# Performance work log

Measured on AMD Instinct MI355X. Metric: run time of the kernel, lower is better.

The kernel has to match this reference:

```python
import jax, jax.numpy as jnp
from jax import lax
import numpy as np

MB, N, QST, EPS = 512, 25, 11, 1e-5

def _coords():
    i = np.arange(25)
    # faithful to python3 true division: (i/5 - 2)/2.0, (i%5 - 2)/2.0
    c = np.stack([(i / 5 - 2) / 2.0, (i % 5 - 2) / 2.0], axis=-1).astype(np.float32)
    return jnp.asarray(c)  # [25, 2]

def _conv_bn(x, w, b, g, beta):
    # Conv2d(k=3, stride=2, pad=1) -> ReLU -> BatchNorm (training-mode batch stats)
    y = lax.conv_general_dilated(x, w, (2, 2), [(1, 1), (1, 1)],
                                 dimension_numbers=('NCHW', 'OIHW', 'NCHW'))
    y = jax.nn.relu(y + b[None, :, None, None])
    mean = y.mean(axis=(0, 2, 3), keepdims=True)
    var = y.var(axis=(0, 2, 3), keepdims=True)
    return (y - mean) * jax.lax.rsqrt(var + EPS) * g[None, :, None, None] + beta[None, :, None, None]

def setup_inputs() -> dict:
    key = jax.random.key(0)
    ks = jax.random.split(key, 20)
    w = lambda k, s: jax.random.normal(k, s, jnp.float32) * 0.05
    inp = {
        'img': jax.random.normal(ks[0], (MB, 3, 75, 75), jnp.float32),
        'qst': jax.random.normal(ks[1], (MB, QST), jnp.float32),
        'c1w': w(ks[2], (24, 3, 3, 3)),  'c1b': jnp.zeros((24,)), 'bn1g': jnp.ones((24,)), 'bn1b': jnp.zeros((24,)),
        'c2w': w(ks[3], (24, 24, 3, 3)), 'c2b': jnp.zeros((24,)), 'bn2g': jnp.ones((24,)), 'bn2b': jnp.zeros((24,)),
        'c3w': w(ks[4], (24, 24, 3, 3)), 'c3b': jnp.zeros((24,)), 'bn3g': jnp.ones((24,)), 'bn3b': jnp.zeros((24,)),
        'c4w': w(ks[5], (24, 24, 3, 3)), 'c4b': jnp.zeros((24,)), 'bn4g': jnp.ones((24,)), 'bn4b': jnp.zeros((24,)),
        'gw1': w(ks[6], (256, 63)),  'gb1': jnp.zeros((256,)),
        'gw2': w(ks[7], (256, 256)), 'gb2': jnp.zeros((256,)),
        'gw3': w(ks[8], (256, 256)), 'gb3': jnp.zeros((256,)),
        'gw4': w(ks[9], (256, 256)), 'gb4': jnp.zeros((256,)),
        'fw1': w(ks[10], (256, 256)), 'fb1': jnp.zeros((256,)),
        'fw2': w(ks[11], (256, 256)), 'fb2': jnp.zeros((256,)),
        'fw3': w(ks[12], (10, 256)),  'fb3': jnp.zeros((10,)),
    }
    return inp

def reference(img, qst, c1w, c1b, bn1g, bn1b, c2w, c2b, bn2g, bn2b,
              c3w, c3b, bn3g, bn3b, c4w, c4b, bn4g, bn4b,
              gw1, gb1, gw2, gb2, gw3, gb3, gw4, gb4,
              fw1, fb1, fw2, fb2, fw3, fb3):
    x = _conv_bn(img, c1w, c1b, bn1g, bn1b)
    x = _conv_bn(x, c2w, c2b, bn2g, bn2b)
    x = _conv_bn(x, c3w, c3b, bn3g, bn3b)
    x = _conv_bn(x, c4w, c4b, bn4g, bn4b)  # [mb, 24, 5, 5]
    mb, C = x.shape[0], x.shape[1]
    n = x.shape[2] * x.shape[3]
    xf = x.reshape(mb, C, n).transpose(0, 2, 1)              # [mb, N, 24]
    coord = jnp.broadcast_to(_coords()[None], (mb, n, 2))
    xf = jnp.concatenate([xf, coord], axis=-1)               # [mb, N, 26]
    qrep = jnp.broadcast_to(qst[:, None, :], (mb, n, QST))
    xj = jnp.concatenate([xf, qrep], axis=-1)                # [mb, N, 37]
    # pair[b,a,c] = [xf[b,c], xf[b,a], qst[b]]  (x_i varies over axis 2, x_j over axis 1)
    pair = jnp.concatenate([
        jnp.broadcast_to(xf[:, None, :, :], (mb, n, n, xf.shape[-1])),
        jnp.broadcast_to(xj[:, :, None, :], (mb, n, n, xj.shape[-1])),
    ], axis=-1)                                              # [mb, N, N, 63]
    h = pair.reshape(mb * n * n, -1)
    for w, b in ((gw1, gb1), (gw2, gb2), (gw3, gb3), (gw4, gb4)):
        h = jax.nn.relu(h @ w.T + b)
    xg = h.reshape(mb, n * n, 256).sum(axis=1)               # sum pooling over pairs
    y = jax.nn.relu(xg @ fw1.T + fb1)
    y = jax.nn.relu(y @ fw2.T + fb2)   # dropout treated as identity (eval mode)
    y = y @ fw3.T + fb3
    return jax.nn.log_softmax(y, axis=-1)
```

## Files before the change

kernel.cpp:

```cpp
#include <hip/hip_runtime.h>

typedef __bf16 bf16_t;
typedef __bf16 bf16x8 __attribute__((ext_vector_type(8)));
typedef __bf16 bf16x4 __attribute__((ext_vector_type(4)));
typedef float f32x16 __attribute__((ext_vector_type(16)));

#define MB 512
#define GROWS 128
#define GT_PER_B 5

__global__ __launch_bounds__(256, 2) void conv1_bn(const float* __restrict__ img,
                                                   const float* __restrict__ wT,
                                                   const float* __restrict__ bias,
                                                   float* __restrict__ out,
                                                   float* __restrict__ statsOut)
{
    __shared__ float in_s[3 * 39 * 77];
    __shared__ float red[48];
    int bid = blockIdx.x;
    int n = bid >> 1, tile = bid & 1;
    int oh0 = tile * 19;
    int tid = threadIdx.x;

    for (int idx = tid; idx < 3 * 39 * 77; idx += 256) {
        int ci = idx / (39 * 77);
        int rem = idx - ci * (39 * 77);
        int r = rem / 77, c = rem - r * 77;
        int ih = 2 * oh0 - 1 + r, iw = c - 1;
        float v = 0.f;
        if ((unsigned)ih < 75u && (unsigned)iw < 75u)
            v = img[((n * 3 + ci) * 75 + ih) * 75 + iw];
        in_s[idx] = v;
    }
    __syncthreads();

    int cg = tid >> 6, lane = tid & 63, co0 = cg * 6;
    int off[12];
    bool pv[12];
#pragma unroll
    for (int j = 0; j < 12; ++j) {
        int p = lane + j * 64;
        pv[j] = p < 722;
        int pc = pv[j] ? p : 0;
        int r0 = pc / 38, c0 = pc - r0 * 38;
        off[j] = (r0 * 2) * 77 + c0 * 2;
    }
    float acc[6][12];
#pragma unroll
    for (int c = 0; c < 6; ++c)
#pragma unroll
        for (int j = 0; j < 12; ++j) acc[c][j] = 0.f;

#pragma unroll 1
    for (int ci = 0; ci < 3; ++ci) {
        const float* ip = in_s + ci * (39 * 77);
        const float* wp = wT + ci * 9 * 24 + co0;
#pragma unroll
        for (int kh = 0; kh < 3; ++kh) {
#pragma unroll
            for (int kw = 0; kw < 3; ++kw) {
                float iv[12];
#pragma unroll
                for (int j = 0; j < 12; ++j) iv[j] = ip[off[j] + kh * 77 + kw];
                const float* wr = wp + (kh * 3 + kw) * 24;
                float2 w01 = *(const float2*)(wr);
                float2 w23 = *(const float2*)(wr + 2);
                float2 w45 = *(const float2*)(wr + 4);
#pragma unroll
                for (int j = 0; j < 12; ++j) {
                    acc[0][j] = fmaf(iv[j], w01.x, acc[0][j]);
                    acc[1][j] = fmaf(iv[j], w01.y, acc[1][j]);
                    acc[2][j] = fmaf(iv[j], w23.x, acc[2][j]);
                    acc[3][j] = fmaf(iv[j], w23.y, acc[3][j]);
                    acc[4][j] = fmaf(iv[j], w45.x, acc[4][j]);
                    acc[5][j] = fmaf(iv[j], w45.y, acc[5][j]);
                }
            }
        }
    }

    float sst[6], sq[6];
#pragma unroll
    for (int c = 0; c < 6; ++c) { sst[c] = 0.f; sq[c] = 0.f; }
#pragma unroll
    for (int c = 0; c < 6; ++c) {
        float bv = bias[co0 + c];
#pragma unroll
        for (int j = 0; j < 12; ++j) {
            if (pv[j]) {
                int p = lane + j * 64;
                int r = p / 38, q = p - r * 38;
                float v = fmaxf(acc[c][j] + bv, 0.f);
                out[((n * 24 + co0 + c) * 38 + oh0 + r) * 38 + q] = v;
                sst[c] += v; sq[c] += v * v;
            }
        }
    }
#pragma unroll
    for (int o = 1; o < 64; o <<= 1) {
#pragma unroll
        for (int c = 0; c < 6; ++c) {
            sst[c] += __shfl_xor(sst[c], o);
            sq[c]  += __shfl_xor(sq[c], o);
        }
    }
    if (lane == 0) {
#pragma unroll
        for (int c = 0; c < 6; ++c) {
            red[(co0 + c) * 2]     = sst[c];
            red[(co0 + c) * 2 + 1] = sq[c];
        }
    }
    __syncthreads();
    if (tid < 48) atomicAdd(&statsOut[tid], red[tid]);
}

template <int HIN, int WIN, int HOUT, int WOUT, int OHT, int NP>
__global__ __launch_bounds__(256, 2) void conv24_bn(const float* __restrict__ in,
                                                    const float* __restrict__ wT,
                                                    const float* __restrict__ bias,
                                                    const float* __restrict__ statsIn,
                                                    const float* __restrict__ gIn,
                                                    const float* __restrict__ bIn, float invcntIn,
                                                    float* __restrict__ out,
                                                    float* __restrict__ statsOut, int tilesPerImg)
{
    constexpr int IR = 2 * OHT + 1;
    constexpr int ICW = 2 * WOUT + 1;
    __shared__ float in_s[24 * IR * ICW];
    __shared__ float aff[48];
    __shared__ float red[48];

    int bid = blockIdx.x;
    int n = bid / tilesPerImg, tile = bid - n * tilesPerImg;
    int oh0 = tile * OHT;
    int tid = threadIdx.x;

    if (tid < 24) {
        float mean = statsIn[tid * 2] * invcntIn;
        float var  = statsIn[tid * 2 + 1] * invcntIn - mean * mean;
        float s    = gIn[tid] * rsqrtf(var + 1e-5f);
        aff[tid * 2] = s;
        aff[tid * 2 + 1] = bIn[tid] - mean * s;
    }
    __syncthreads();
    for (int idx = tid; idx < 24 * IR * ICW; idx += 256) {
        int ci = idx / (IR * ICW);
        int rem = idx - ci * (IR * ICW);
        int r = rem / ICW, c = rem - r * ICW;
        int ih = 2 * oh0 - 1 + r, iw = c - 1;
        float v = 0.f;
        if ((unsigned)ih < (unsigned)HIN && (unsigned)iw < (unsigned)WIN)
            v = aff[ci * 2] * in[((n * 24 + ci) * HIN + ih) * WIN + iw] + aff[ci * 2 + 1];
        in_s[idx] = v;
    }
    __syncthreads();

    int cg = tid >> 6, lane = tid & 63, co0 = cg * 6;
    int nvr = HOUT - oh0; if (nvr > OHT) nvr = OHT;
    int nposv = nvr * WOUT;
    int off[NP];
    bool pv[NP];
#pragma unroll
    for (int j = 0; j < NP; ++j) {
        int p = lane + j * 64;
        pv[j] = p < nposv;
        int pc = pv[j] ? p : 0;
        int r0 = pc / WOUT, c0 = pc - r0 * WOUT;
        off[j] = (r0 * 2) * ICW + c0 * 2;
    }
    float acc[6][NP];
#pragma unroll
    for (int c = 0; c < 6; ++c)
#pragma unroll
        for (int j = 0; j < NP; ++j) acc[c][j] = 0.f;

#pragma unroll 1
    for (int ci = 0; ci < 24; ++ci) {
        const float* ip = in_s + ci * (IR * ICW);
        const float* wp = wT + ci * 9 * 24 + co0;
#pragma unroll
        for (int kh = 0; kh < 3; ++kh) {
#pragma unroll
            for (int kw = 0; kw < 3; ++kw) {
                float iv[NP];
#pragma unroll
                for (int j = 0; j < NP; ++j) iv[j] = ip[off[j] + kh * ICW + kw];
                const float* wr = wp + (kh * 3 + kw) * 24;
                float2 w01 = *(const float2*)(wr);
                float2 w23 = *(const float2*)(wr + 2);
                float2 w45 = *(const float2*)(wr + 4);
#pragma unroll
                for (int j = 0; j < NP; ++j) {
                    acc[0][j] = fmaf(iv[j], w01.x, acc[0][j]);
                    acc[1][j] = fmaf(iv[j], w01.y, acc[1][j]);
                    acc[2][j] = fmaf(iv[j], w23.x, acc[2][j]);
                    acc[3][j] = fmaf(iv[j], w23.y, acc[3][j]);
                    acc[4][j] = fmaf(iv[j], w45.x, acc[4][j]);
                    acc[5][j] = fmaf(iv[j], w45.y, acc[5][j]);
                }
            }
        }
    }

    float sst[6], sq[6];
#pragma unroll
    for (int c = 0; c < 6; ++c) { sst[c] = 0.f; sq[c] = 0.f; }
#pragma unroll
    for (int c = 0; c < 6; ++c) {
        float bv = bias[co0 + c];
#pragma unroll
        for (int j = 0; j < NP; ++j) {
            if (pv[j]) {
                int p = lane + j * 64;
                int r = p / WOUT, q = p - r * WOUT;
                float v = fmaxf(acc[c][j] + bv, 0.f);
                out[((n * 24 + co0 + c) * HOUT + oh0 + r) * WOUT + q] = v;
                sst[c] += v; sq[c] += v * v;
            }
        }
    }
#pragma unroll
    for (int o = 1; o < 64; o <<= 1) {
#pragma unroll
        for (int c = 0; c < 6; ++c) {
            sst[c] += __shfl_xor(sst[c], o);
            sq[c]  += __shfl_xor(sq[c], o);
        }
    }
    if (lane == 0) {
#pragma unroll
        for (int c = 0; c < 6; ++c) {
            red[(co0 + c) * 2]     = sst[c];
            red[(co0 + c) * 2 + 1] = sq[c];
        }
    }
    __syncthreads();
    if (tid < 48) atomicAdd(&statsOut[tid], red[tid]);
}

__global__ void build_features(const float* __restrict__ y4, const float* __restrict__ stats4,
                               const float* __restrict__ g4, const float* __restrict__ b4,
                               const float* __restrict__ qst,
                               bf16_t* __restrict__ xf26, bf16_t* __restrict__ qstb)
{
    int idx = blockIdx.x * 256 + threadIdx.x;
    if (idx < MB * 11) qstb[idx] = (bf16_t)qst[idx];
    if (idx >= MB * 25) return;
    int b = idx / 25, p = idx % 25;
    const float invcnt = 1.f / (MB * 25);
#pragma unroll
    for (int ch = 0; ch < 24; ++ch) {
        float mean = stats4[ch * 2] * invcnt;
        float var  = stats4[ch * 2 + 1] * invcnt - mean * mean;
        float s    = g4[ch] * rsqrtf(var + 1e-5f);
        float v    = s * y4[(b * 24 + ch) * 25 + p] + (b4[ch] - mean * s);
        xf26[idx * 26 + ch] = (bf16_t)v;
    }
    xf26[idx * 26 + 24] = (bf16_t)((p / 5.0f - 2.0f) * 0.5f);
    xf26[idx * 26 + 25] = (bf16_t)(((float)(p % 5) - 2.0f) * 0.5f);
}

__device__ __forceinline__ void frag256(int idx, const float* __restrict__ gw, bf16_t* __restrict__ Wf)
{
    int j = idx & 7, lane = (idx >> 3) & 63, ks = (idx >> 9) & 15, nt = idx >> 13;
    int n = nt * 32 + (lane & 31), k = ks * 16 + (lane >> 5) * 8 + j;
    Wf[idx] = (bf16_t)gw[n * 256 + k];
}

__global__ void prep_weights(const float* __restrict__ gw1, const float* __restrict__ gw2,
                             const float* __restrict__ gw3, const float* __restrict__ gw4,
                             const float* __restrict__ fw1, const float* __restrict__ fw2,
                             const float* __restrict__ c1w, const float* __restrict__ c2w,
                             const float* __restrict__ c3w, const float* __restrict__ c4w,
                             bf16_t* __restrict__ W1f, bf16_t* __restrict__ W2f,
                             bf16_t* __restrict__ W3f, bf16_t* __restrict__ W4f,
                             float* __restrict__ fw1T, float* __restrict__ fw2T,
                             float* __restrict__ wT1, float* __restrict__ wT2,
                             float* __restrict__ wT3, float* __restrict__ wT4)
{
    int idx = blockIdx.x * 256 + threadIdx.x;
    if (idx < 16384) {
        int j = idx & 7, lane = (idx >> 3) & 63, ks = (idx >> 9) & 3, nt = idx >> 11;
        int n = nt * 32 + (lane & 31), k = ks * 16 + (lane >> 5) * 8 + j;
        W1f[idx] = (k < 63) ? (bf16_t)gw1[n * 63 + k] : (bf16_t)0.0f;
        return;
    }
    idx -= 16384;
    if (idx < 65536) { frag256(idx, gw2, W2f); return; }
    idx -= 65536;
    if (idx < 65536) { frag256(idx, gw3, W3f); return; }
    idx -= 65536;
    if (idx < 65536) { frag256(idx, gw4, W4f); return; }
    idx -= 65536;
    if (idx < 65536) { int k = idx >> 8, nn = idx & 255; fw1T[idx] = fw1[nn * 256 + k]; return; }
    idx -= 65536;
    if (idx < 65536) { int k = idx >> 8, nn = idx & 255; fw2T[idx] = fw2[nn * 256 + k]; return; }
    idx -= 65536;
    if (idx < 648)   { int k = idx / 24, co = idx - k * 24; wT1[idx] = c1w[co * 27 + k]; return; }
    idx -= 648;
    if (idx < 5184)  { int k = idx / 24, co = idx - k * 24; wT2[idx] = c2w[co * 216 + k]; return; }
    idx -= 5184;
    if (idx < 5184)  { int k = idx / 24, co = idx - k * 24; wT3[idx] = c3w[co * 216 + k]; return; }
    idx -= 5184;
    if (idx < 5184)  { int k = idx / 24, co = idx - k * 24; wT4[idx] = c4w[co * 216 + k]; return; }
}


template <int NKS>
__device__ __forceinline__ void g_layer(const bf16_t* hs, const bf16_t* __restrict__ Wf,
                                        int wid, int lane, f32x16 acc[4][2])
{
    int m31 = lane & 31, half = lane >> 5;
#pragma unroll
    for (int mt = 0; mt < 4; ++mt)
#pragma unroll
        for (int nt = 0; nt < 2; ++nt) acc[mt][nt] = (f32x16)(0.f);
#pragma unroll
    for (int ks = 0; ks < NKS; ++ks) {
        int kc = ks * 2 + half;
        bf16x8 hf[4];
#pragma unroll
        for (int mt = 0; mt < 4; ++mt) {
            int m = mt * 32 + m31;
            hf[mt] = *(const bf16x8*)(hs + m * 256 + ((kc ^ m31) << 3));
        }
        bf16x8 wf[2];
#pragma unroll
        for (int nt = 0; nt < 2; ++nt)
            wf[nt] = *(const bf16x8*)(Wf + (size_t)(((wid * 2 + nt) * NKS + ks) * 64 + lane) * 8);
#pragma unroll
        for (int nt = 0; nt < 2; ++nt)
#pragma unroll
            for (int mt = 0; mt < 4; ++mt)
                acc[mt][nt] = __builtin_amdgcn_mfma_f32_32x32x16_bf16(wf[nt], hf[mt], acc[mt][nt], 0, 0, 0);
    }
}

__device__ __forceinline__ void g_store(bf16_t* hs, const float* __restrict__ bias,
                                        int wid, int lane, f32x16 acc[4][2])
{
    int m31 = lane & 31, half = lane >> 5;
#pragma unroll
    for (int mt = 0; mt < 4; ++mt) {
        int m = mt * 32 + m31;
#pragma unroll
        for (int nt = 0; nt < 2; ++nt) {
            int nbase = (wid * 2 + nt) * 32;
#pragma unroll
            for (int g = 0; g < 4; ++g) {
                int n0 = nbase + g * 8 + half * 4;
                float4 bv = *(const float4*)(bias + n0);
                bf16x4 v;
                v[0] = (bf16_t)fmaxf(acc[mt][nt][g * 4 + 0] + bv.x, 0.f);
                v[1] = (bf16_t)fmaxf(acc[mt][nt][g * 4 + 1] + bv.y, 0.f);
                v[2] = (bf16_t)fmaxf(acc[mt][nt][g * 4 + 2] + bv.z, 0.f);
                v[3] = (bf16_t)fmaxf(acc[mt][nt][g * 4 + 3] + bv.w, 0.f);
                int chunk = n0 >> 3;
                *(bf16x4*)(hs + m * 256 + ((chunk ^ m31) << 3) + (half << 2)) = v;
            }
        }
    }
}

__global__ void __launch_bounds__(256, 2)
g_mlp(const bf16_t* __restrict__ xf26, const bf16_t* __restrict__ qstb,
      const bf16_t* __restrict__ W1f, const bf16_t* __restrict__ W2f,
      const bf16_t* __restrict__ W3f, const bf16_t* __restrict__ W4f,
      const float* __restrict__ b1, const float* __restrict__ b2,
      const float* __restrict__ b3, const float* __restrict__ b4,
      float* __restrict__ xg)
{
    __shared__ __align__(16) bf16_t hs[GROWS * 256];
    int b    = blockIdx.x / GT_PER_B;
    int tile = blockIdx.x % GT_PER_B;
    int tid  = threadIdx.x;

    for (int i = tid; i < GROWS * 8; i += 256) {
        int m = i >> 3, c = i & 7;
        int p = tile * GROWS + m;
        bf16x8 v;
        if (p < 625) {
            int a = p / 25, cp = p - a * 25;
            const bf16_t* f1 = xf26 + (b * 25 + cp) * 26;
            const bf16_t* f2 = xf26 + (b * 25 + a) * 26;
            const bf16_t* f3 = qstb + b * 11;
#pragma unroll
            for (int j = 0; j < 8; ++j) {
                int col = c * 8 + j;
                bf16_t u = (bf16_t)0.0f;
                if (col < 26) u = f1[col];
                else if (col < 52) u = f2[col - 26];
                else if (col < 63) u = f3[col - 52];
                v[j] = u;
            }
        } else {
#pragma unroll
            for (int j = 0; j < 8; ++j) v[j] = (bf16_t)0.0f;
        }
        *(bf16x8*)(hs + m * 256 + ((c ^ (m & 31)) << 3)) = v;
    }
    __syncthreads();

    int wid = tid >> 6, lane = tid & 63;
    int m31 = lane & 31, half = lane >> 5;
    f32x16 acc[4][2];

    g_layer<4>(hs, W1f, wid, lane, acc);
    __syncthreads(); g_store(hs, b1, wid, lane, acc); __syncthreads();
    g_layer<16>(hs, W2f, wid, lane, acc);
    __syncthreads(); g_store(hs, b2, wid, lane, acc); __syncthreads();
    g_layer<16>(hs, W3f, wid, lane, acc);
    __syncthreads(); g_store(hs, b3, wid, lane, acc); __syncthreads();
    g_layer<16>(hs, W4f, wid, lane, acc);

#pragma unroll
    for (int nt = 0; nt < 2; ++nt) {
        int nbase = (wid * 2 + nt) * 32;
        float bf[16];
#pragma unroll
        for (int r = 0; r < 16; ++r)
            bf[r] = b4[nbase + (r & 3) + 8 * (r >> 2) + 4 * half];
        f32x16 t = (f32x16)(0.f);
#pragma unroll
        for (int mt = 0; mt < 4; ++mt) {
            int p = tile * GROWS + mt * 32 + m31;
            if (p < 625) {
#pragma unroll
                for (int r = 0; r < 16; ++r)
                    t[r] += fmaxf(acc[mt][nt][r] + bf[r], 0.f);
            }
        }
#pragma unroll
        for (int off = 1; off < 32; off <<= 1) {
#pragma unroll
            for (int r = 0; r < 16; ++r) t[r] += __shfl_xor(t[r], off);
        }
        if (m31 == 0) {
#pragma unroll
            for (int r = 0; r < 16; ++r) {
                int nn = nbase + (r & 3) + 8 * (r >> 2) + 4 * half;
                atomicAdd(&xg[b * 256 + nn], t[r]);
            }
        }
    }
}

__global__ void f_mlp(const float* __restrict__ xg, const float* __restrict__ fw1T, const float* __restrict__ fb1,
                      const float* __restrict__ fw2T, const float* __restrict__ fb2,
                      const float* __restrict__ fw3, const float* __restrict__ fb3,
                      float* __restrict__ out)
{
    __shared__ float xa[256], xb[256], lg[10];
    int b = blockIdx.x, t = threadIdx.x;
    xa[t] = xg[b * 256 + t];
    __syncthreads();
    float a = fb1[t];
    for (int k = 0; k < 256; ++k) a += fw1T[k * 256 + t] * xa[k];
    xb[t] = fmaxf(a, 0.f);
    __syncthreads();
    a = fb2[t];
    for (int k = 0; k < 256; ++k) a += fw2T[k * 256 + t] * xb[k];
    xa[t] = fmaxf(a, 0.f);
    __syncthreads();
    if (t < 10) {
        float s = fb3[t];
        for (int k = 0; k < 256; ++k) s += fw3[t * 256 + k] * xa[k];
        lg[t] = s;
    }
    __syncthreads();
    if (t == 0) {
        float m = lg[0];
        for (int i = 1; i < 10; ++i) m = fmaxf(m, lg[i]);
        float s = 0.f;
        for (int i = 0; i < 10; ++i) s += expf(lg[i] - m);
        float ls = m + logf(s);
        for (int i = 0; i < 10; ++i) out[b * 10 + i] = lg[i] - ls;
    }
}

extern "C" void kernel_launch(void* const* d_in, const int* in_sizes, int n_in,
                              void* d_out, int out_size, void* d_ws, size_t ws_size,
                              hipStream_t stream)
{
    (void)in_sizes; (void)n_in; (void)out_size; (void)ws_size;
    const float* img  = (const float*)d_in[0];
    const float* qst  = (const float*)d_in[1];
    const float* c1w  = (const float*)d_in[2];
    const float* c1b  = (const float*)d_in[3];
    const float* bn1g = (const float*)d_in[4];
    const float* bn1b = (const float*)d_in[5];
    const float* c2w  = (const float*)d_in[6];
    const float* c2b  = (const float*)d_in[7];
    const float* bn2g = (const float*)d_in[8];
    const float* bn2b = (const float*)d_in[9];
    const float* c3w  = (const float*)d_in[10];
    const float* c3b  = (const float*)d_in[11];
    const float* bn3g = (const float*)d_in[12];
    const float* bn3b = (const float*)d_in[13];
    const float* c4w  = (const float*)d_in[14];
    const float* c4b  = (const float*)d_in[15];
    const float* bn4g = (const float*)d_in[16];
    const float* bn4b = (const float*)d_in[17];
    const float* gw1  = (const float*)d_in[18];
    const float* gb1  = (const float*)d_in[19];
    const float* gw2  = (const float*)d_in[20];
    const float* gb2  = (const float*)d_in[21];
    const float* gw3  = (const float*)d_in[22];
    const float* gb3  = (const float*)d_in[23];
    const float* gw4  = (const float*)d_in[24];
    const float* gb4  = (const float*)d_in[25];
    const float* fw1  = (const float*)d_in[26];
    const float* fb1  = (const float*)d_in[27];
    const float* fw2  = (const float*)d_in[28];
    const float* fb2  = (const float*)d_in[29];
    const float* fw3  = (const float*)d_in[30];
    const float* fb3  = (const float*)d_in[31];

    const int Y1 = 512 * 24 * 38 * 38;
    const int Y2 = 512 * 24 * 19 * 19;
    const int Y3 = 512 * 24 * 10 * 10;
    const int Y4 = 512 * 24 * 5 * 5;

    float* fp = (float*)d_ws;
    float* y1    = fp;  fp += Y1;
    float* y2    = fp;  fp += Y2;
    float* y3    = fp;  fp += Y3;
    float* y4    = fp;  fp += Y4;
    float* stats = fp;  fp += 192;
    float* xg    = fp;  fp += 512 * 256;
    float* fw1T  = fp;  fp += 65536;
    float* fw2T  = fp;  fp += 65536;
    float* wT1   = fp;  fp += 648;
    float* wT2   = fp;  fp += 5184;
    float* wT3   = fp;  fp += 5184;
    float* wT4   = fp;  fp += 5184;
    bf16_t* bp   = (bf16_t*)fp;
    bf16_t* xf26 = bp;  bp += 512 * 25 * 26;
    bf16_t* qstb = bp;  bp += 512 * 11;
    bf16_t* W1f  = bp;  bp += 16384;
    bf16_t* W2f  = bp;  bp += 65536;
    bf16_t* W3f  = bp;  bp += 65536;
    bf16_t* W4f  = bp;  bp += 65536;

    hipMemsetAsync(stats, 0, 192 * sizeof(float), stream);
    hipMemsetAsync(xg, 0, 512 * 256 * sizeof(float), stream);

    prep_weights<<<1408, 256, 0, stream>>>(gw1, gw2, gw3, gw4, fw1, fw2, c1w, c2w, c3w, c4w,
                                           W1f, W2f, W3f, W4f, fw1T, fw2T,
                                           wT1, wT2, wT3, wT4);

    conv1_bn<<<1024, 256, 0, stream>>>(img, wT1, c1b, y1, stats + 0);

    conv24_bn<38, 38, 19, 19, 5, 2><<<2048, 256, 0, stream>>>(
        y1, wT2, c2b, stats + 0, bn1g, bn1b, 1.f / (512.f * 1444.f),
        y2, stats + 48, 4);

    conv24_bn<19, 19, 10, 10, 10, 2><<<512, 256, 0, stream>>>(
        y2, wT3, c3b, stats + 48, bn2g, bn2b, 1.f / (512.f * 361.f),
        y3, stats + 96, 1);

    conv24_bn<10, 10, 5, 5, 5, 1><<<512, 256, 0, stream>>>(
        y3, wT4, c4b, stats + 96, bn3g, bn3b, 1.f / (512.f * 100.f),
        y4, stats + 144, 1);

    build_features<<<50, 256, 0, stream>>>(y4, stats + 144, bn4g, bn4b, qst, xf26, qstb);

    g_mlp<<<512 * GT_PER_B, 256, 0, stream>>>(xf26, qstb, W1f, W2f, W3f, W4f,
                                              gb1, gb2, gb3, gb4, xg);

    f_mlp<<<512, 256, 0, stream>>>(xg, fw1T, fb1, fw2T, fb2, fw3, fb3, (float*)d_out);
}
```

Baseline: 601.4 us.

## Replace conv kernels with per-thread-position double-buffered conv and retile g_mlp

The four convolution kernels are replaced by one templated kernel in which each thread owns a single output position and accumulates all 24 output channels. Input channels are staged one at a time into a double-buffered shared slab instead of loading every channel at once. The g_mlp row tile shrinks from 128 to 96 rows (7 tiles per sample instead of 5), with occupancy hinted at 3 blocks per SM. The aim is less shared memory, more overlap, and higher occupancy, at the cost of a barrier per input channel, more redundant weight loads per thread, and more g_mlp blocks and atomics.

```diff
diff --git a/kernel.cpp b/kernel.cpp
--- a/kernel.cpp
+++ b/kernel.cpp
@@ -6,237 +6,116 @@
 typedef float f32x16 __attribute__((ext_vector_type(16)));
 
 #define MB 512
-#define GROWS 128
-#define GT_PER_B 5
-
-__global__ __launch_bounds__(256, 2) void conv1_bn(const float* __restrict__ img,
-                                                   const float* __restrict__ wT,
-                                                   const float* __restrict__ bias,
-                                                   float* __restrict__ out,
-                                                   float* __restrict__ statsOut)
-{
-    __shared__ float in_s[3 * 39 * 77];
-    __shared__ float red[48];
-    int bid = blockIdx.x;
-    int n = bid >> 1, tile = bid & 1;
-    int oh0 = tile * 19;
-    int tid = threadIdx.x;
-
-    for (int idx = tid; idx < 3 * 39 * 77; idx += 256) {
-        int ci = idx / (39 * 77);
-        int rem = idx - ci * (39 * 77);
-        int r = rem / 77, c = rem - r * 77;
-        int ih = 2 * oh0 - 1 + r, iw = c - 1;
-        float v = 0.f;
-        if ((unsigned)ih < 75u && (unsigned)iw < 75u)
-            v = img[((n * 3 + ci) * 75 + ih) * 75 + iw];
-        in_s[idx] = v;
-    }
-    __syncthreads();
-
-    int cg = tid >> 6, lane = tid & 63, co0 = cg * 6;
-    int off[12];
-    bool pv[12];
-#pragma unroll
-    for (int j = 0; j < 12; ++j) {
-        int p = lane + j * 64;
-        pv[j] = p < 722;
-        int pc = pv[j] ? p : 0;
-        int r0 = pc / 38, c0 = pc - r0 * 38;
-        off[j] = (r0 * 2) * 77 + c0 * 2;
-    }
-    float acc[6][12];
-#pragma unroll
-    for (int c = 0; c < 6; ++c)
-#pragma unroll
-        for (int j = 0; j < 12; ++j) acc[c][j] = 0.f;
-
-#pragma unroll 1
-    for (int ci = 0; ci < 3; ++ci) {
-        const float* ip = in_s + ci * (39 * 77);
-        const float* wp = wT + ci * 9 * 24 + co0;
-#pragma unroll
-        for (int kh = 0; kh < 3; ++kh) {
-#pragma unroll
-            for (int kw = 0; kw < 3; ++kw) {
-                float iv[12];
-#pragma unroll
-                for (int j = 0; j < 12; ++j) iv[j] = ip[off[j] + kh * 77 + kw];
-                const float* wr = wp + (kh * 3 + kw) * 24;
-                float2 w01 = *(const float2*)(wr);
-                float2 w23 = *(const float2*)(wr + 2);
-                float2 w45 = *(const float2*)(wr + 4);
-#pragma unroll
-                for (int j = 0; j < 12; ++j) {
-                    acc[0][j] = fmaf(iv[j], w01.x, acc[0][j]);
-                    acc[1][j] = fmaf(iv[j], w01.y, acc[1][j]);
-                    acc[2][j] = fmaf(iv[j], w23.x, acc[2][j]);
-                    acc[3][j] = fmaf(iv[j], w23.y, acc[3][j]);
-                    acc[4][j] = fmaf(iv[j], w45.x, acc[4][j]);
-                    acc[5][j] = fmaf(iv[j], w45.y, acc[5][j]);
-                }
-            }
-        }
-    }
-
-    float sst[6], sq[6];
-#pragma unroll
-    for (int c = 0; c < 6; ++c) { sst[c] = 0.f; sq[c] = 0.f; }
-#pragma unroll
-    for (int c = 0; c < 6; ++c) {
-        float bv = bias[co0 + c];
-#pragma unroll
-        for (int j = 0; j < 12; ++j) {
-            if (pv[j]) {
-                int p = lane + j * 64;
-                int r = p / 38, q = p - r * 38;
-                float v = fmaxf(acc[c][j] + bv, 0.f);
-                out[((n * 24 + co0 + c) * 38 + oh0 + r) * 38 + q] = v;
-                sst[c] += v; sq[c] += v * v;
-            }
-        }
-    }
-#pragma unroll
-    for (int o = 1; o < 64; o <<= 1) {
-#pragma unroll
-        for (int c = 0; c < 6; ++c) {
-            sst[c] += __shfl_xor(sst[c], o);
-            sq[c]  += __shfl_xor(sq[c], o);
-        }
-    }
-    if (lane == 0) {
-#pragma unroll
-        for (int c = 0; c < 6; ++c) {
-            red[(co0 + c) * 2]     = sst[c];
-            red[(co0 + c) * 2 + 1] = sq[c];
-        }
-    }
-    __syncthreads();
-    if (tid < 48) atomicAdd(&statsOut[tid], red[tid]);
-}
-
-template <int HIN, int WIN, int HOUT, int WOUT, int OHT, int NP>
-__global__ __launch_bounds__(256, 2) void conv24_bn(const float* __restrict__ in,
-                                                    const float* __restrict__ wT,
-                                                    const float* __restrict__ bias,
-                                                    const float* __restrict__ statsIn,
-                                                    const float* __restrict__ gIn,
-                                                    const float* __restrict__ bIn, float invcntIn,
-                                                    float* __restrict__ out,
-                                                    float* __restrict__ statsOut, int tilesPerImg)
-{
-    constexpr int IR = 2 * OHT + 1;
+#define GROWS 96
+#define GT_PER_B 7
+
+template <int CIN, int HIN, int WIN, int HOUT, int WOUT, int OHT, int BLK>
+__global__ __launch_bounds__(BLK) void conv_v2(const float* __restrict__ in,
+                                               const float* __restrict__ wT,
+                                               const float* __restrict__ bias,
+                                               const float* __restrict__ statsIn,
+                                               const float* __restrict__ gIn,
+                                               const float* __restrict__ bIn, float invcntIn,
+                                               float* __restrict__ out,
+                                               float* __restrict__ statsOut, int tilesPerImg)
+{
+    constexpr int IR  = 2 * OHT + 1;
     constexpr int ICW = 2 * WOUT + 1;
-    __shared__ float in_s[24 * IR * ICW];
-    __shared__ float aff[48];
-    __shared__ float red[48];
+    constexpr int NW  = BLK / 64;
+    __shared__ float slab[2][IR * ICW];
+    __shared__ float aff[CIN * 2];
+    __shared__ float red[NW * 48];
 
     int bid = blockIdx.x;
     int n = bid / tilesPerImg, tile = bid - n * tilesPerImg;
     int oh0 = tile * OHT;
     int tid = threadIdx.x;
 
-    if (tid < 24) {
-        float mean = statsIn[tid * 2] * invcntIn;
-        float var  = statsIn[tid * 2 + 1] * invcntIn - mean * mean;
-        float s    = gIn[tid] * rsqrtf(var + 1e-5f);
-        aff[tid * 2] = s;
-        aff[tid * 2 + 1] = bIn[tid] - mean * s;
-    }
-    __syncthreads();
-    for (int idx = tid; idx < 24 * IR * ICW; idx += 256) {
-        int ci = idx / (IR * ICW);
-        int rem = idx - ci * (IR * ICW);
-        int r = rem / ICW, c = rem - r * ICW;
-        int ih = 2 * oh0 - 1 + r, iw = c - 1;
-        float v = 0.f;
-        if ((unsigned)ih < (unsigned)HIN && (unsigned)iw < (unsigned)WIN)
-            v = aff[ci * 2] * in[((n * 24 + ci) * HIN + ih) * WIN + iw] + aff[ci * 2 + 1];
-        in_s[idx] = v;
-    }
-    __syncthreads();
-
-    int cg = tid >> 6, lane = tid & 63, co0 = cg * 6;
+    if (tid < CIN) {
+        if (statsIn) {
+            float mean = statsIn[tid * 2] * invcntIn;
+            float var  = statsIn[tid * 2 + 1] * invcntIn - mean * mean;
+            float s    = gIn[tid] * rsqrtf(var + 1e-5f);
+            aff[tid * 2] = s;
+            aff[tid * 2 + 1] = bIn[tid] - mean * s;
+        } else {
+            aff[tid * 2] = 1.f;
+            aff[tid * 2 + 1] = 0.f;
+        }
+    }
+    __syncthreads();
+
+    auto stage = [&](int ci, float* buf) {
+        float sc = aff[ci * 2], sh = aff[ci * 2 + 1];
+        const float* src = in + ((size_t)(n * CIN + ci) * HIN) * WIN;
+        for (int idx = tid; idx < IR * ICW; idx += BLK) {
+            int rr = idx / ICW, cc = idx - rr * ICW;
+            int ih = 2 * oh0 - 1 + rr, iw = cc - 1;
+            float v = 0.f;
+            if ((unsigned)ih < (unsigned)HIN && (unsigned)iw < (unsigned)WIN)
+                v = fmaf(src[ih * WIN + iw], sc, sh);
+            buf[idx] = v;
+        }
+    };
+
     int nvr = HOUT - oh0; if (nvr > OHT) nvr = OHT;
-    int nposv = nvr * WOUT;
-    int off[NP];
-    bool pv[NP];
-#pragma unroll
-    for (int j = 0; j < NP; ++j) {
-        int p = lane + j * 64;
-        pv[j] = p < nposv;
-        int pc = pv[j] ? p : 0;
-        int r0 = pc / WOUT, c0 = pc - r0 * WOUT;
-        off[j] = (r0 * 2) * ICW + c0 * 2;
-    }
-    float acc[6][NP];
-#pragma unroll
-    for (int c = 0; c < 6; ++c)
-#pragma unroll
-        for (int j = 0; j < NP; ++j) acc[c][j] = 0.f;
+    int npos = nvr * WOUT;
+    bool valid = tid < npos;
+    int pc = valid ? tid : 0;
+    int r = pc / WOUT, q = pc - r * WOUT;
+
+    float acc[24];
+#pragma unroll
+    for (int c = 0; c < 24; ++c) acc[c] = 0.f;
+
+    stage(0, slab[0]);
+    __syncthreads();
 
 #pragma unroll 1
-    for (int ci = 0; ci < 24; ++ci) {
-        const float* ip = in_s + ci * (IR * ICW);
-        const float* wp = wT + ci * 9 * 24 + co0;
-#pragma unroll
-        for (int kh = 0; kh < 3; ++kh) {
-#pragma unroll
-            for (int kw = 0; kw < 3; ++kw) {
-                float iv[NP];
-#pragma unroll
-                for (int j = 0; j < NP; ++j) iv[j] = ip[off[j] + kh * ICW + kw];
-                const float* wr = wp + (kh * 3 + kw) * 24;
-                float2 w01 = *(const float2*)(wr);
-                float2 w23 = *(const float2*)(wr + 2);
-                float2 w45 = *(const float2*)(wr + 4);
-#pragma unroll
-                for (int j = 0; j < NP; ++j) {
-                    acc[0][j] = fmaf(iv[j], w01.x, acc[0][j]);
-                    acc[1][j] = fmaf(iv[j], w01.y, acc[1][j]);
-                    acc[2][j] = fmaf(iv[j], w23.x, acc[2][j]);
-                    acc[3][j] = fmaf(iv[j], w23.y, acc[3][j]);
-                    acc[4][j] = fmaf(iv[j], w45.x, acc[4][j]);
-                    acc[5][j] = fmaf(iv[j], w45.y, acc[5][j]);
-                }
+    for (int ci = 0; ci < CIN; ++ci) {
+        const float* sp = slab[ci & 1];
+        if (ci + 1 < CIN) stage(ci + 1, slab[(ci + 1) & 1]);
+        const float* wp = wT + ci * 9 * 24;
+        float iv[9];
+#pragma unroll
+        for (int t = 0; t < 9; ++t)
+            iv[t] = sp[(2 * r + t / 3) * ICW + 2 * q + t % 3];
+#pragma unroll
+        for (int t = 0; t < 9; ++t) {
+#pragma unroll
+            for (int c4 = 0; c4 < 6; ++c4) {
+                float4 w4 = *(const float4*)(wp + t * 24 + c4 * 4);
+                acc[c4 * 4 + 0] = fmaf(iv[t], w4.x, acc[c4 * 4 + 0]);
+                acc[c4 * 4 + 1] = fmaf(iv[t], w4.y, acc[c4 * 4 + 1]);
+                acc[c4 * 4 + 2] = fmaf(iv[t], w4.z, acc[c4 * 4 + 2]);
+                acc[c4 * 4 + 3] = fmaf(iv[t], w4.w, acc[c4 * 4 + 3]);
             }
         }
-    }
-
-    float sst[6], sq[6];
-#pragma unroll
-    for (int c = 0; c < 6; ++c) { sst[c] = 0.f; sq[c] = 0.f; }
-#pragma unroll
-    for (int c = 0; c < 6; ++c) {
-        float bv = bias[co0 + c];
-#pragma unroll
-        for (int j = 0; j < NP; ++j) {
-            if (pv[j]) {
-                int p = lane + j * 64;
-                int r = p / WOUT, q = p - r * WOUT;
-                float v = fmaxf(acc[c][j] + bv, 0.f);
-                out[((n * 24 + co0 + c) * HOUT + oh0 + r) * WOUT + q] = v;
-                sst[c] += v; sq[c] += v * v;
-            }
-        }
-    }
-#pragma unroll
-    for (int o = 1; o < 64; o <<= 1) {
-#pragma unroll
-        for (int c = 0; c < 6; ++c) {
-            sst[c] += __shfl_xor(sst[c], o);
-            sq[c]  += __shfl_xor(sq[c], o);
-        }
-    }
-    if (lane == 0) {
-#pragma unroll
-        for (int c = 0; c < 6; ++c) {
-            red[(co0 + c) * 2]     = sst[c];
-            red[(co0 + c) * 2 + 1] = sq[c];
-        }
-    }
-    __syncthreads();
-    if (tid < 48) atomicAdd(&statsOut[tid], red[tid]);
+        __syncthreads();
+    }
+
+    int wv = tid >> 6, lane = tid & 63;
+#pragma unroll
+    for (int c = 0; c < 24; ++c) {
+        float v = fmaxf(acc[c] + bias[c], 0.f);
+        if (!valid) v = 0.f;
+        if (valid)
+            out[((size_t)(n * 24 + c) * HOUT + oh0 + r) * WOUT + q] = v;
+        float s1 = v, s2 = v * v;
+#pragma unroll
+        for (int o = 1; o < 64; o <<= 1) {
+            s1 += __shfl_xor(s1, o);
+            s2 += __shfl_xor(s2, o);
+        }
+        if (lane == 0) { red[wv * 48 + c * 2] = s1; red[wv * 48 + c * 2 + 1] = s2; }
+    }
+    __syncthreads();
+    if (tid < 48) {
+        float t = 0.f;
+#pragma unroll
+        for (int w = 0; w < NW; ++w) t += red[w * 48 + tid];
+        atomicAdd(&statsOut[tid], t);
+    }
 }
 
 __global__ void build_features(const float* __restrict__ y4, const float* __restrict__ stats4,
@@ -309,19 +188,19 @@
 
 template <int NKS>
 __device__ __forceinline__ void g_layer(const bf16_t* hs, const bf16_t* __restrict__ Wf,
-                                        int wid, int lane, f32x16 acc[4][2])
+                                        int wid, int lane, f32x16 acc[3][2])
 {
     int m31 = lane & 31, half = lane >> 5;
 #pragma unroll
-    for (int mt = 0; mt < 4; ++mt)
+    for (int mt = 0; mt < 3; ++mt)
 #pragma unroll
         for (int nt = 0; nt < 2; ++nt) acc[mt][nt] = (f32x16)(0.f);
 #pragma unroll
     for (int ks = 0; ks < NKS; ++ks) {
         int kc = ks * 2 + half;
-        bf16x8 hf[4];
-#pragma unroll
-        for (int mt = 0; mt < 4; ++mt) {
+        bf16x8 hf[3];
+#pragma unroll
+        for (int mt = 0; mt < 3; ++mt) {
             int m = mt * 32 + m31;
             hf[mt] = *(const bf16x8*)(hs + m * 256 + ((kc ^ m31) << 3));
         }
@@ -332,17 +211,17 @@
 #pragma unroll
         for (int nt = 0; nt < 2; ++nt)
 #pragma unroll
-            for (int mt = 0; mt < 4; ++mt)
+            for (int mt = 0; mt < 3; ++mt)
                 acc[mt][nt] = __builtin_amdgcn_mfma_f32_32x32x16_bf16(wf[nt], hf[mt], acc[mt][nt], 0, 0, 0);
     }
 }
 
 __device__ __forceinline__ void g_store(bf16_t* hs, const float* __restrict__ bias,
-                                        int wid, int lane, f32x16 acc[4][2])
+                                        int wid, int lane, f32x16 acc[3][2])
 {
     int m31 = lane & 31, half = lane >> 5;
 #pragma unroll
-    for (int mt = 0; mt < 4; ++mt) {
+    for (int mt = 0; mt < 3; ++mt) {
         int m = mt * 32 + m31;
 #pragma unroll
         for (int nt = 0; nt < 2; ++nt) {
@@ -363,7 +242,7 @@
     }
 }
 
-__global__ void __launch_bounds__(256, 2)
+__global__ void __launch_bounds__(256, 3)
 g_mlp(const bf16_t* __restrict__ xf26, const bf16_t* __restrict__ qstb,
       const bf16_t* __restrict__ W1f, const bf16_t* __restrict__ W2f,
       const bf16_t* __restrict__ W3f, const bf16_t* __restrict__ W4f,
@@ -404,7 +283,7 @@
 
     int wid = tid >> 6, lane = tid & 63;
     int m31 = lane & 31, half = lane >> 5;
-    f32x16 acc[4][2];
+    f32x16 acc[3][2];
 
     g_layer<4>(hs, W1f, wid, lane, acc);
     __syncthreads(); g_store(hs, b1, wid, lane, acc); __syncthreads();
@@ -423,7 +302,7 @@
             bf[r] = b4[nbase + (r & 3) + 8 * (r >> 2) + 4 * half];
         f32x16 t = (f32x16)(0.f);
 #pragma unroll
-        for (int mt = 0; mt < 4; ++mt) {
+        for (int mt = 0; mt < 3; ++mt) {
             int p = tile * GROWS + mt * 32 + m31;
             if (p < 625) {
 #pragma unroll
@@ -550,19 +429,17 @@
                                            W1f, W2f, W3f, W4f, fw1T, fw2T,
                                            wT1, wT2, wT3, wT4);
 
-    conv1_bn<<<1024, 256, 0, stream>>>(img, wT1, c1b, y1, stats + 0);
-
-    conv24_bn<38, 38, 19, 19, 5, 2><<<2048, 256, 0, stream>>>(
-        y1, wT2, c2b, stats + 0, bn1g, bn1b, 1.f / (512.f * 1444.f),
-        y2, stats + 48, 4);
-
-    conv24_bn<19, 19, 10, 10, 10, 2><<<512, 256, 0, stream>>>(
-        y2, wT3, c3b, stats + 48, bn2g, bn2b, 1.f / (512.f * 361.f),
-        y3, stats + 96, 1);
-
-    conv24_bn<10, 10, 5, 5, 5, 1><<<512, 256, 0, stream>>>(
-        y3, wT4, c4b, stats + 96, bn3g, bn3b, 1.f / (512.f * 100.f),
-        y4, stats + 144, 1);
+    conv_v2<3, 75, 75, 38, 38, 10, 384><<<512 * 4, 384, 0, stream>>>(
+        img, wT1, c1b, nullptr, nullptr, nullptr, 0.f, y1, stats + 0, 4);
+
+    conv_v2<24, 38, 38, 19, 19, 10, 192><<<512 * 2, 192, 0, stream>>>(
+        y1, wT2, c2b, stats + 0, bn1g, bn1b, 1.f / (512.f * 1444.f), y2, stats + 48, 2);
+
+    conv_v2<24, 19, 19, 10, 10, 10, 128><<<512, 128, 0, stream>>>(
+        y2, wT3, c3b, stats + 48, bn2g, bn2b, 1.f / (512.f * 361.f), y3, stats + 96, 1);
+
+    conv_v2<24, 10, 10, 5, 5, 5, 64><<<512, 64, 0, stream>>>(
+        y3, wT4, c4b, stats + 96, bn3g, bn3b, 1.f / (512.f * 100.f), y4, stats + 144, 1);
 
     build_features<<<50, 256, 0, stream>>>(y4, stats + 144, bn4g, bn4b, qst, xf26, qstb);
 
```

New measurement: 616.9 us. +2.6%, slower.
